# Kernel optimization log

Measured on AMD Instinct MI355X. Metric: run time of the kernel, lower is better.

## Reference

```python
import jax, jax.numpy as jnp
import numpy as np

N = 10000   # nodes
E = 80000   # edges
B = 2       # batch
T = 12      # time steps
F_IN = 64
F_OUT = 64


def setup_inputs() -> dict:
    key = jax.random.key(0)
    ks = jax.random.split(key, 8)
    x = jax.random.normal(ks[0], (B, N, T, F_IN), dtype=jnp.float32)
    src = jax.random.randint(ks[1], (E,), 0, N)
    dst = jax.random.randint(ks[2], (E,), 0, N)
    s = 1.0 / np.sqrt(F_IN)
    W_pool = jax.random.uniform(ks[3], (F_IN, F_IN), jnp.float32, -s, s)
    b_pool = jax.random.uniform(ks[4], (F_IN,), jnp.float32, -s, s)
    W_neigh = jax.random.uniform(ks[5], (F_OUT, F_IN), jnp.float32, -s, s)
    W_self = jax.random.uniform(ks[6], (F_OUT, F_IN), jnp.float32, -s, s)
    bias = jnp.zeros((F_OUT,), jnp.float32)
    return dict(x=x, src=src, dst=dst, W_pool=W_pool, b_pool=b_pool,
                W_neigh=W_neigh, W_self=W_self, bias=bias)


def reference(x, src, dst, W_pool, b_pool, W_neigh, W_self, bias):
    # x: (B, N, T, F) -> (N, B, T, F); node dim first as SAGEConv expects
    h = jnp.transpose(x, (1, 0, 2, 3))
    # pool aggregator: per-node MLP + relu (done on nodes, then gathered per edge
    # -- identical math to gather-then-MLP since the MLP is per-node/elementwise)
    msg = jax.nn.relu(jnp.einsum('nbtf,gf->nbtg', h, W_pool) + b_pool)  # (N,B,T,F)
    m = msg[src]                                                        # (E,B,T,F) gather
    neigh = jax.ops.segment_max(m, dst, num_segments=N)                 # max-pool per dst node
    # zero-in-degree nodes get -inf from segment_max -> replace with 0 (DGL behavior)
    neigh = jnp.where(jnp.isfinite(neigh), neigh, jnp.zeros((), neigh.dtype))
    rst = (jnp.einsum('nbtf,of->nbto', h, W_self)
           + jnp.einsum('nbtf,of->nbto', neigh, W_neigh)
           + bias)                                                      # (N,B,T,F_OUT)
    return jnp.transpose(rst, (1, 0, 2, 3))                              # (B,N,T,F_OUT)
```

## Files before the change

kernel.cpp:

```cpp
#include <hip/hip_runtime.h>

#define NN 10000
#define NE 80000
#define NB 2
#define NT 12
#define NF 64
#define ROWS (NB*NN*NT)

typedef __attribute__((ext_vector_type(8))) short bf16x8;
typedef __attribute__((ext_vector_type(4))) float f32x4;

__device__ __forceinline__ unsigned short f2b(float f) {
    unsigned int u = __builtin_bit_cast(unsigned int, f);
    u += 0x7fffu + ((u >> 16) & 1u);
    return (unsigned short)(u >> 16);
}
__device__ __forceinline__ float b2f_lo(unsigned int u){ return __builtin_bit_cast(float, u << 16); }
__device__ __forceinline__ float b2f_hi(unsigned int u){ return __builtin_bit_cast(float, u & 0xffff0000u); }

__global__ __launch_bounds__(256) void k_prep(const float* __restrict__ Wp,
        const float* __restrict__ Wn, const float* __restrict__ Ws,
        unsigned short* __restrict__ Wp_b, unsigned short* __restrict__ Wcat) {
    int t = threadIdx.x;
    for (int i = t; i < 4096; i += 256) {
        Wp_b[i] = f2b(Wp[i]);
        int o = i >> 6, g = i & 63;
        Wcat[o*128 + g] = f2b(Ws[i]);
        Wcat[o*128 + 64 + ((g & 15)*4 + (g >> 4))] = f2b(Wn[i]);
    }
}

__global__ __launch_bounds__(256) void k_msg(const float* __restrict__ x,
        const unsigned short* __restrict__ Wp_b, const float* __restrict__ bp,
        unsigned short* __restrict__ msg, unsigned short* __restrict__ xb) {
    __shared__ __align__(16) unsigned short A[128*72];
    __shared__ __align__(16) unsigned short W[64*72];
    int tid = threadIdx.x;
    {
        int row = tid >> 2, c = (tid & 3) * 16;
        bf16x8 w0 = *(const bf16x8*)(Wp_b + row*64 + c);
        bf16x8 w1 = *(const bf16x8*)(Wp_b + row*64 + c + 8);
        *(bf16x8*)(W + row*72 + c)     = w0;
        *(bf16x8*)(W + row*72 + c + 8) = w1;
    }
    int m0 = blockIdx.x * 128;
    #pragma unroll
    for (int k = 0; k < 8; ++k) {
        int c = tid + 256*k;
        int row = c >> 4, f0 = (c & 15) * 4;
        float4 v = *(const float4*)(x + (size_t)(m0 + row)*64 + f0);
        uint2 p;
        p.x = f2b(v.x) | ((unsigned int)f2b(v.y) << 16);
        p.y = f2b(v.z) | ((unsigned int)f2b(v.w) << 16);
        *(uint2*)(A + row*72 + f0) = p;
        *(uint2*)(xb + (size_t)(m0 + row)*64 + f0) = p;
    }
    __syncthreads();

    int lane = tid & 63, w = tid >> 6;
    int cl = lane & 15, gq = lane >> 4;
    f32x4 acc[2][4] = {};
    #pragma unroll
    for (int kk = 0; kk < 2; ++kk) {
        int ko = kk*32 + gq*8;
        bf16x8 a0 = *(const bf16x8*)(A + (w*32 + cl)*72 + ko);
        bf16x8 a1 = *(const bf16x8*)(A + (w*32 + 16 + cl)*72 + ko);
        #pragma unroll
        for (int nf = 0; nf < 4; ++nf) {
            bf16x8 b = *(const bf16x8*)(W + (nf*16 + cl)*72 + ko);
            acc[0][nf] = __builtin_amdgcn_mfma_f32_16x16x32_bf16(a0, b, acc[0][nf], 0,0,0);
            acc[1][nf] = __builtin_amdgcn_mfma_f32_16x16x32_bf16(a1, b, acc[1][nf], 0,0,0);
        }
    }
    float bpv[4];
    #pragma unroll
    for (int nf = 0; nf < 4; ++nf) bpv[nf] = bp[nf*16 + cl];
    #pragma unroll
    for (int m = 0; m < 2; ++m)
    #pragma unroll
    for (int r = 0; r < 4; ++r) {
        int row = m0 + w*32 + m*16 + gq*4 + r;
        float v0 = fmaxf(acc[m][0][r] + bpv[0], 0.f);
        float v1 = fmaxf(acc[m][1][r] + bpv[1], 0.f);
        float v2 = fmaxf(acc[m][2][r] + bpv[2], 0.f);
        float v3 = fmaxf(acc[m][3][r] + bpv[3], 0.f);
        uint2 p;
        p.x = f2b(v0) | ((unsigned int)f2b(v1) << 16);
        p.y = f2b(v2) | ((unsigned int)f2b(v3) << 16);
        *(uint2*)(msg + (size_t)row*64 + cl*4) = p;
    }
}

__global__ void k_count(const int* __restrict__ dst, int* __restrict__ cnt) {
    int e = blockIdx.x * blockDim.x + threadIdx.x;
    if (e < NE) atomicAdd(&cnt[dst[e]], 1);
}

__global__ __launch_bounds__(1024) void k_scan(const int* __restrict__ cnt,
        int* __restrict__ rowptr, int* __restrict__ wofs) {
    __shared__ int s[1024];
    int tid = threadIdx.x;
    const int C = 10;
    int base = tid * C;
    int loc[C];
    int sum = 0;
    for (int i = 0; i < C; ++i) {
        int idx = base + i;
        int v = (idx < NN) ? cnt[idx] : 0;
        loc[i] = sum;
        sum += v;
    }
    s[tid] = sum;
    __syncthreads();
    for (int off = 1; off < 1024; off <<= 1) {
        int v = (tid >= off) ? s[tid - off] : 0;
        __syncthreads();
        s[tid] += v;
        __syncthreads();
    }
    int prev = (tid == 0) ? 0 : s[tid - 1];
    for (int i = 0; i < C; ++i) {
        int idx = base + i;
        if (idx < NN) {
            int v = prev + loc[i];
            rowptr[idx] = v;
            wofs[idx]   = v;
        }
    }
    if (tid == 1023) rowptr[NN] = s[1023];
}

__global__ void k_scatter(const int* __restrict__ src, const int* __restrict__ dst,
        int* __restrict__ wofs, int* __restrict__ csr) {
    int e = blockIdx.x * blockDim.x + threadIdx.x;
    if (e < NE) {
        int pos = atomicAdd(&wofs[dst[e]], 1);
        csr[pos] = src[e];
    }
}

__global__ __launch_bounds__(256) void k_out(const unsigned short* __restrict__ xb,
        const unsigned short* __restrict__ msg, const unsigned short* __restrict__ Wcat,
        const float* __restrict__ bias,
        const int* __restrict__ rowptr, const int* __restrict__ csr,
        float* __restrict__ out) {
    __shared__ __align__(16) unsigned short A[32*136];
    __shared__ __align__(16) unsigned short W[64*136];
    int tid = threadIdx.x;
    int n = blockIdx.x;

    #pragma unroll
    for (int k = 0; k < 4; ++k) {
        int c = tid + 256*k;
        int row = c >> 4, f0 = (c & 15) * 8;
        *(bf16x8*)(W + row*136 + f0) = *(const bf16x8*)(Wcat + row*128 + f0);
    }
    {
        int c = tid, row = c >> 4, f0 = (c & 15) * 4;
        int b = row / 12, tt = row - b*12;
        *(uint2*)(A + row*136 + f0) =
            *(const uint2*)(xb + ((size_t)(b*NN + n)*12 + tt)*64 + f0);
        if (tid < 128) {
            c = tid + 256; row = c >> 4; f0 = (c & 15)*4;
            b = row / 12; tt = row - b*12;
            *(uint2*)(A + row*136 + f0) =
                *(const uint2*)(xb + ((size_t)(b*NN + n)*12 + tt)*64 + f0);
        }
    }
    const unsigned int* msg_dw = (const unsigned int*)msg;
    int rp0 = rowptr[n], rp1 = rowptr[n + 1];
    int base[3], dsto[3];
    #pragma unroll
    for (int k = 0; k < 3; ++k) {
        int i = tid + 256*k;
        int b = i / 384, rem = i - b*384;
        int tt = rem >> 5, f2 = rem & 31;
        base[k] = b * (NN*384) + rem;
        dsto[k] = (b*12 + tt)*136 + 64 + f2*2;
    }
    float mlo[3] = {0.f,0.f,0.f}, mhi[3] = {0.f,0.f,0.f};
    int e = rp0;
    for (; e + 1 < rp1; e += 2) {
        int s0 = csr[e] * 384, s1 = csr[e+1] * 384;
        #pragma unroll
        for (int k = 0; k < 3; ++k) {
            unsigned int u0 = msg_dw[base[k] + s0];
            unsigned int u1 = msg_dw[base[k] + s1];
            mlo[k] = fmaxf(fmaxf(mlo[k], b2f_lo(u0)), b2f_lo(u1));
            mhi[k] = fmaxf(fmaxf(mhi[k], b2f_hi(u0)), b2f_hi(u1));
        }
    }
    if (e < rp1) {
        int s0 = csr[e] * 384;
        #pragma unroll
        for (int k = 0; k < 3; ++k) {
            unsigned int u0 = msg_dw[base[k] + s0];
            mlo[k] = fmaxf(mlo[k], b2f_lo(u0));
            mhi[k] = fmaxf(mhi[k], b2f_hi(u0));
        }
    }
    #pragma unroll
    for (int k = 0; k < 3; ++k) {
        unsigned int lo = __builtin_bit_cast(unsigned int, mlo[k]) >> 16;
        unsigned int hi = __builtin_bit_cast(unsigned int, mhi[k]) & 0xffff0000u;
        *(unsigned int*)(A + dsto[k]) = hi | lo;
    }
    __syncthreads();

    int lane = tid & 63, w = tid >> 6;
    int cl = lane & 15, gq = lane >> 4;
    f32x4 acc0 = {}, acc1 = {};
    #pragma unroll
    for (int kk = 0; kk < 4; ++kk) {
        int ko = kk*32 + gq*8;
        bf16x8 a0 = *(const bf16x8*)(A + cl*136 + ko);
        bf16x8 a1 = *(const bf16x8*)(A + (16 + cl)*136 + ko);
        bf16x8 b  = *(const bf16x8*)(W + (w*16 + cl)*136 + ko);
        acc0 = __builtin_amdgcn_mfma_f32_16x16x32_bf16(a0, b, acc0, 0,0,0);
        acc1 = __builtin_amdgcn_mfma_f32_16x16x32_bf16(a1, b, acc1, 0,0,0);
    }
    float bv = bias[w*16 + cl];
    #pragma unroll
    for (int r = 0; r < 4; ++r) {
        int row = gq*4 + r;
        int b0 = row / 12, tt = row - b0*12;
        out[((size_t)(b0*NN + n)*12 + tt)*64 + w*16 + cl] = acc0[r] + bv;
    }
    if (gq < 2) {
        #pragma unroll
        for (int r = 0; r < 4; ++r) {
            int row = 16 + gq*4 + r;
            int b0 = row / 12, tt = row - b0*12;
            out[((size_t)(b0*NN + n)*12 + tt)*64 + w*16 + cl] = acc1[r] + bv;
        }
    }
}

extern "C" void kernel_launch(void* const* d_in, const int* in_sizes, int n_in,
                              void* d_out, int out_size, void* d_ws, size_t ws_size,
                              hipStream_t stream) {
    const float* x    = (const float*)d_in[0];
    const int*   src  = (const int*)  d_in[1];
    const int*   dst  = (const int*)  d_in[2];
    const float* Wp   = (const float*)d_in[3];
    const float* bp   = (const float*)d_in[4];
    const float* Wn   = (const float*)d_in[5];
    const float* Wsf  = (const float*)d_in[6];
    const float* bias = (const float*)d_in[7];
    float* out = (float*)d_out;

    char* ws = (char*)d_ws;
    int*            cnt    = (int*)           (ws);
    int*            rowptr = (int*)           (ws + 40064);
    int*            wofs   = (int*)           (ws + 80128);
    int*            csr    = (int*)           (ws + 120192);
    unsigned short* Wp_b   = (unsigned short*)(ws + 440320);
    unsigned short* Wcat   = (unsigned short*)(ws + 448512);
    unsigned short* msg    = (unsigned short*)(ws + 464896);
    unsigned short* xb     = (unsigned short*)(ws + 31184896);

    hipMemsetAsync(cnt, 0, NN * sizeof(int), stream);
    k_prep   <<<1, 256, 0, stream>>>(Wp, Wn, Wsf, Wp_b, Wcat);
    k_msg    <<<ROWS/128, 256, 0, stream>>>(x, Wp_b, bp, msg, xb);
    k_count  <<<(NE + 255) / 256, 256, 0, stream>>>(dst, cnt);
    k_scan   <<<1, 1024, 0, stream>>>(cnt, rowptr, wofs);
    k_scatter<<<(NE + 255) / 256, 256, 0, stream>>>(src, dst, wofs, csr);
    k_out    <<<NN, 256, 0, stream>>>(xb, msg, Wcat, bias, rowptr, csr, out);
}
```

Before: 105.4 us.

## Store messages node-major, unroll gather by four, read weights from global

The message buffer is now written node-major, with both batches and all time steps of a node contiguous (768 dwords). Each neighbor gather therefore reads one contiguous 3 KB row instead of two strided halves. The gather loop is unrolled by four edges to keep more loads in flight. The weight matrix is no longer staged in shared memory; MFMA B operands are loaded straight from global/L2, and the unused A rows are zeroed. Dropping the weight stage cuts LDS use and the copy work, and launch_bounds(256,8) asks for higher occupancy, at the cost of more global weight reads per block.

```diff
diff --git a/kernel.cpp b/kernel.cpp
--- a/kernel.cpp
+++ b/kernel.cpp
@@ -80,6 +80,9 @@
     #pragma unroll
     for (int r = 0; r < 4; ++r) {
         int row = m0 + w*32 + m*16 + gq*4 + r;
+        int b  = row / (NN*NT);
+        int rem = row - b*(NN*NT);
+        int node = rem / NT, t = rem - node*NT;
         float v0 = fmaxf(acc[m][0][r] + bpv[0], 0.f);
         float v1 = fmaxf(acc[m][1][r] + bpv[1], 0.f);
         float v2 = fmaxf(acc[m][2][r] + bpv[2], 0.f);
@@ -87,7 +90,7 @@
         uint2 p;
         p.x = f2b(v0) | ((unsigned int)f2b(v1) << 16);
         p.y = f2b(v2) | ((unsigned int)f2b(v3) << 16);
-        *(uint2*)(msg + (size_t)row*64 + cl*4) = p;
+        *(uint2*)(msg + ((size_t)(node*24 + b*12 + t)*64) + cl*4) = p;
     }
 }
 
@@ -139,71 +142,67 @@
     }
 }
 
-__global__ __launch_bounds__(256) void k_out(const unsigned short* __restrict__ xb,
+__global__ __launch_bounds__(256, 8) void k_out(const unsigned short* __restrict__ xb,
         const unsigned short* __restrict__ msg, const unsigned short* __restrict__ Wcat,
         const float* __restrict__ bias,
         const int* __restrict__ rowptr, const int* __restrict__ csr,
         float* __restrict__ out) {
     __shared__ __align__(16) unsigned short A[32*136];
-    __shared__ __align__(16) unsigned short W[64*136];
     int tid = threadIdx.x;
     int n = blockIdx.x;
 
-    #pragma unroll
-    for (int k = 0; k < 4; ++k) {
-        int c = tid + 256*k;
-        int row = c >> 4, f0 = (c & 15) * 8;
-        *(bf16x8*)(W + row*136 + f0) = *(const bf16x8*)(Wcat + row*128 + f0);
-    }
     {
         int c = tid, row = c >> 4, f0 = (c & 15) * 4;
         int b = row / 12, tt = row - b*12;
         *(uint2*)(A + row*136 + f0) =
             *(const uint2*)(xb + ((size_t)(b*NN + n)*12 + tt)*64 + f0);
         if (tid < 128) {
-            c = tid + 256; row = c >> 4; f0 = (c & 15)*4;
-            b = row / 12; tt = row - b*12;
-            *(uint2*)(A + row*136 + f0) =
-                *(const uint2*)(xb + ((size_t)(b*NN + n)*12 + tt)*64 + f0);
+            int c2 = tid + 256, row2 = c2 >> 4, f02 = (c2 & 15)*4;
+            int b2 = row2 / 12, tt2 = row2 - b2*12;
+            *(uint2*)(A + row2*136 + f02) =
+                *(const uint2*)(xb + ((size_t)(b2*NN + n)*12 + tt2)*64 + f02);
+        } else {
+            unsigned int* z = (unsigned int*)(A + 24*136);
+            int i = tid - 128;
+            #pragma unroll
+            for (int k = 0; k < 5; ++k) { int j = i + 128*k; if (j < 544) z[j] = 0u; }
         }
     }
     const unsigned int* msg_dw = (const unsigned int*)msg;
     int rp0 = rowptr[n], rp1 = rowptr[n + 1];
-    int base[3], dsto[3];
-    #pragma unroll
-    for (int k = 0; k < 3; ++k) {
-        int i = tid + 256*k;
-        int b = i / 384, rem = i - b*384;
-        int tt = rem >> 5, f2 = rem & 31;
-        base[k] = b * (NN*384) + rem;
-        dsto[k] = (b*12 + tt)*136 + 64 + f2*2;
-    }
+    int i0 = tid, i1 = tid + 256, i2 = tid + 512;
     float mlo[3] = {0.f,0.f,0.f}, mhi[3] = {0.f,0.f,0.f};
     int e = rp0;
-    for (; e + 1 < rp1; e += 2) {
-        int s0 = csr[e] * 384, s1 = csr[e+1] * 384;
-        #pragma unroll
-        for (int k = 0; k < 3; ++k) {
-            unsigned int u0 = msg_dw[base[k] + s0];
-            unsigned int u1 = msg_dw[base[k] + s1];
-            mlo[k] = fmaxf(fmaxf(mlo[k], b2f_lo(u0)), b2f_lo(u1));
-            mhi[k] = fmaxf(fmaxf(mhi[k], b2f_hi(u0)), b2f_hi(u1));
-        }
-    }
-    if (e < rp1) {
-        int s0 = csr[e] * 384;
-        #pragma unroll
-        for (int k = 0; k < 3; ++k) {
-            unsigned int u0 = msg_dw[base[k] + s0];
-            mlo[k] = fmaxf(mlo[k], b2f_lo(u0));
-            mhi[k] = fmaxf(mhi[k], b2f_hi(u0));
-        }
-    }
-    #pragma unroll
-    for (int k = 0; k < 3; ++k) {
-        unsigned int lo = __builtin_bit_cast(unsigned int, mlo[k]) >> 16;
-        unsigned int hi = __builtin_bit_cast(unsigned int, mhi[k]) & 0xffff0000u;
-        *(unsigned int*)(A + dsto[k]) = hi | lo;
+    for (; e + 4 <= rp1; e += 4) {
+        int s0 = csr[e]*768, s1 = csr[e+1]*768, s2 = csr[e+2]*768, s3 = csr[e+3]*768;
+        unsigned int u00 = msg_dw[s0+i0], u01 = msg_dw[s0+i1], u02 = msg_dw[s0+i2];
+        unsigned int u10 = msg_dw[s1+i0], u11 = msg_dw[s1+i1], u12 = msg_dw[s1+i2];
+        unsigned int u20 = msg_dw[s2+i0], u21 = msg_dw[s2+i1], u22 = msg_dw[s2+i2];
+        unsigned int u30 = msg_dw[s3+i0], u31 = msg_dw[s3+i1], u32 = msg_dw[s3+i2];
+        mlo[0] = fmaxf(fmaxf(fmaxf(mlo[0], b2f_lo(u00)), fmaxf(b2f_lo(u10), b2f_lo(u20))), b2f_lo(u30));
+        mhi[0] = fmaxf(fmaxf(fmaxf(mhi[0], b2f_hi(u00)), fmaxf(b2f_hi(u10), b2f_hi(u20))), b2f_hi(u30));
+        mlo[1] = fmaxf(fmaxf(fmaxf(mlo[1], b2f_lo(u01)), fmaxf(b2f_lo(u11), b2f_lo(u21))), b2f_lo(u31));
+        mhi[1] = fmaxf(fmaxf(fmaxf(mhi[1], b2f_hi(u01)), fmaxf(b2f_hi(u11), b2f_hi(u21))), b2f_hi(u31));
+        mlo[2] = fmaxf(fmaxf(fmaxf(mlo[2], b2f_lo(u02)), fmaxf(b2f_lo(u12), b2f_lo(u22))), b2f_lo(u32));
+        mhi[2] = fmaxf(fmaxf(fmaxf(mhi[2], b2f_hi(u02)), fmaxf(b2f_hi(u12), b2f_hi(u22))), b2f_hi(u32));
+    }
+    for (; e < rp1; ++e) {
+        int s0 = csr[e]*768;
+        unsigned int u0 = msg_dw[s0+i0], u1 = msg_dw[s0+i1], u2 = msg_dw[s0+i2];
+        mlo[0] = fmaxf(mlo[0], b2f_lo(u0));  mhi[0] = fmaxf(mhi[0], b2f_hi(u0));
+        mlo[1] = fmaxf(mlo[1], b2f_lo(u1));  mhi[1] = fmaxf(mhi[1], b2f_hi(u1));
+        mlo[2] = fmaxf(mlo[2], b2f_lo(u2));  mhi[2] = fmaxf(mhi[2], b2f_hi(u2));
+    }
+    {
+        unsigned int lo0 = __builtin_bit_cast(unsigned int, mlo[0]) >> 16;
+        unsigned int hi0 = __builtin_bit_cast(unsigned int, mhi[0]) & 0xffff0000u;
+        *(unsigned int*)(A + (i0>>5)*136 + 64 + (i0&31)*2) = hi0 | lo0;
+        unsigned int lo1 = __builtin_bit_cast(unsigned int, mlo[1]) >> 16;
+        unsigned int hi1 = __builtin_bit_cast(unsigned int, mhi[1]) & 0xffff0000u;
+        *(unsigned int*)(A + (i1>>5)*136 + 64 + (i1&31)*2) = hi1 | lo1;
+        unsigned int lo2 = __builtin_bit_cast(unsigned int, mlo[2]) >> 16;
+        unsigned int hi2 = __builtin_bit_cast(unsigned int, mhi[2]) & 0xffff0000u;
+        *(unsigned int*)(A + (i2>>5)*136 + 64 + (i2&31)*2) = hi2 | lo2;
     }
     __syncthreads();
 
@@ -213,9 +212,9 @@
     #pragma unroll
     for (int kk = 0; kk < 4; ++kk) {
         int ko = kk*32 + gq*8;
+        bf16x8 b  = *(const bf16x8*)(Wcat + (w*16 + cl)*128 + ko);
         bf16x8 a0 = *(const bf16x8*)(A + cl*136 + ko);
         bf16x8 a1 = *(const bf16x8*)(A + (16 + cl)*136 + ko);
-        bf16x8 b  = *(const bf16x8*)(W + (w*16 + cl)*136 + ko);
         acc0 = __builtin_amdgcn_mfma_f32_16x16x32_bf16(a0, b, acc0, 0,0,0);
         acc1 = __builtin_amdgcn_mfma_f32_16x16x32_bf16(a1, b, acc1, 0,0,0);
     }
```

New measurement: 107.4 us. Within noise of the previous version (+1.9%).
